# Optimization experiments

Hardware: AMD Instinct MI355X
Metric: run time of the kernel (lower is better)

## Reference

```python
import jax, jax.numpy as jnp
import numpy as np

EPS = 1e-5

@jax.custom_vjp
def sign_ste(x):
    # binarize to {-1, +1}; sign(0) maps to +1 as in most binary-net impls
    return jnp.where(x >= 0, 1.0, -1.0).astype(x.dtype)

def _sign_fwd(x):
    return sign_ste(x), x

def _sign_bwd(x, g):
    # straight-through estimator with hardtanh clipping
    return (g * (jnp.abs(x) <= 1.0).astype(g.dtype),)

sign_ste.defvjp(_sign_fwd, _sign_bwd)


def setup_inputs() -> dict:
    key = jax.random.key(0)
    k1, k2, k3 = jax.random.split(key, 3)
    N, Cin, Cout = 65536, 1024, 1024
    return {
        "x": jax.random.normal(k1, (N, Cin), dtype=jnp.float32),
        "gamma": jnp.ones((Cin,), dtype=jnp.float32),
        "beta": jnp.zeros((Cin,), dtype=jnp.float32),
        "W": jax.random.normal(k2, (Cout, Cin), dtype=jnp.float32) * 0.03,
        "b": jnp.zeros((Cout,), dtype=jnp.float32),
        "scale": jnp.ones((Cout,), dtype=jnp.float32),
        "alpha": jnp.float32(0.25),
    }


def reference(x, gamma, beta, W, b, scale, alpha):
    # 1) BatchNorm1d centering (training-mode batch statistics over nodes)
    mu = jnp.mean(x, axis=0)
    var = jnp.var(x, axis=0)
    xh = (x - mu) * jax.lax.rsqrt(var + EPS) * gamma + beta
    # 2) STE binarize activations
    xq = sign_ste(xh)
    # 3) binary linear: sign(W) GEMM + bias  -> [N, Cout]
    wq = sign_ste(W)
    y = jnp.einsum('nc,oc->no', xq, wq) + b
    # 4) learned per-channel rescale
    y = y * scale
    # 5) PReLU
    return jnp.where(y > 0, y, alpha * y)
```

## Files before the change

kernel.cpp:

```cpp
#include <hip/hip_runtime.h>
#include <stdint.h>
#include <math.h>

#define NROWS 65536
#define CIN   1024
#define COUT  1024
#define BN_EPS 1e-5


static constexpr size_t OFF_PSUM = 0;
static constexpr size_t OFF_PSQ  = 4ull * 1024 * 1024;
static constexpr size_t OFF_MU   = 8ull * 1024 * 1024;
static constexpr size_t OFF_INV  = 8ull * 1024 * 1024 + 4096;
static constexpr size_t OFF_WB   = 9ull * 1024 * 1024;
static constexpr size_t OFF_AB   = 10ull * 1024 * 1024;

typedef uint64_t u64x2 __attribute__((ext_vector_type(2)));
typedef uint32_t u32x4 __attribute__((ext_vector_type(4)));

__global__ __launch_bounds__(256) void k_stats_partial(
    const float* __restrict__ x, double* __restrict__ psum, double* __restrict__ psq) {
  int tid = threadIdx.x;
  size_t r0 = (size_t)blockIdx.x * 128;
  const float4* xp = (const float4*)x + r0 * 256 + tid;
  double s0 = 0, s1 = 0, s2 = 0, s3 = 0;
  double q0 = 0, q1 = 0, q2 = 0, q3 = 0;
  for (int r = 0; r < 128; r += 8) {
    float4 v[8];
#pragma unroll
    for (int u = 0; u < 8; ++u) v[u] = xp[(size_t)(r + u) * 256];
#pragma unroll
    for (int u = 0; u < 8; ++u) {
      double a = (double)v[u].x, b = (double)v[u].y;
      double c = (double)v[u].z, d = (double)v[u].w;
      s0 += a; q0 = fma(a, a, q0);
      s1 += b; q1 = fma(b, b, q1);
      s2 += c; q2 = fma(c, c, q2);
      s3 += d; q3 = fma(d, d, q3);
    }
  }
  size_t base = (size_t)blockIdx.x * CIN + (size_t)tid * 4;
  double2* ps = (double2*)(psum + base);
  ps[0] = make_double2(s0, s1);
  ps[1] = make_double2(s2, s3);
  double2* pq = (double2*)(psq + base);
  pq[0] = make_double2(q0, q1);
  pq[1] = make_double2(q2, q3);
}

__global__ __launch_bounds__(256) void k_stats_final(
    const double* __restrict__ psum, const double* __restrict__ psq,
    float* __restrict__ mu, float* __restrict__ inv) {
  __shared__ double sd[16][16];
  __shared__ double sq[16][16];
  int tid = threadIdx.x;
  int cl = tid & 15;
  int g  = tid >> 4;
  int col = blockIdx.x * 16 + cl;
  double s = 0, q = 0;
  for (int i = 0; i < 32; ++i) {
    size_t chunk = (size_t)(g * 32 + i);
    s += psum[chunk * CIN + col];
    q += psq [chunk * CIN + col];
  }
  sd[g][cl] = s;
  sq[g][cl] = q;
  __syncthreads();
  if (tid < 16) {
    s = 0; q = 0;
#pragma unroll
    for (int i = 0; i < 16; ++i) { s += sd[i][tid]; q += sq[i][tid]; }
    double mean = s / (double)NROWS;
    double var  = q / (double)NROWS - mean * mean;
    int c = blockIdx.x * 16 + tid;
    mu[c]  = (float)mean;
    inv[c] = (float)(1.0 / sqrt(var + (double)BN_EPS));
  }
}

__global__ __launch_bounds__(256) void k_binarize_x(
    const float* __restrict__ x, const float* __restrict__ mu,
    const float* __restrict__ inv, const float* __restrict__ gamma,
    const float* __restrict__ beta, uint64_t* __restrict__ Abits) {
  int tid = threadIdx.x, lane = tid & 63, wv = tid >> 6;
  float4 M  = ((const float4*)mu)[tid];
  float4 I  = ((const float4*)inv)[tid];
  float4 G  = ((const float4*)gamma)[tid];
  float4 Bt = ((const float4*)beta)[tid];
  size_t n0 = (size_t)blockIdx.x * 8;
  const float4* xp = (const float4*)x + n0 * 256 + tid;
  for (int r = 0; r < 8; ++r) {
    float4 v = xp[(size_t)r * 256];
    float h0 = ((v.x - M.x) * I.x) * G.x + Bt.x;
    float h1 = ((v.y - M.y) * I.y) * G.y + Bt.y;
    float h2 = ((v.z - M.z) * I.z) * G.z + Bt.z;
    float h3 = ((v.w - M.w) * I.w) * G.w + Bt.w;
    uint64_t b0 = __ballot(h0 >= 0.0f);
    uint64_t b1 = __ballot(h1 >= 0.0f);
    uint64_t b2 = __ballot(h2 >= 0.0f);
    uint64_t b3 = __ballot(h3 >= 0.0f);
    uint64_t t0 = b0, t1 = b1;
    if (lane == 1) { t0 = b2; t1 = b3; }
    if (lane < 2) {
      u64x2 val; val.x = t0; val.y = t1;
      *(u64x2*)(Abits + (n0 + r) * 16 + wv * 4 + lane * 2) = val;
    }
  }
}

__global__ __launch_bounds__(256) void k_binarize_w(
    const float* __restrict__ W, uint64_t* __restrict__ Wbits) {
  int tid = threadIdx.x, lane = tid & 63, wv = tid >> 6;
  size_t o0 = (size_t)blockIdx.x * 8;
  const float4* wp = (const float4*)W + o0 * 256 + tid;
  for (int r = 0; r < 8; ++r) {
    float4 v = wp[(size_t)r * 256];
    uint64_t b0 = __ballot(v.x >= 0.0f);
    uint64_t b1 = __ballot(v.y >= 0.0f);
    uint64_t b2 = __ballot(v.z >= 0.0f);
    uint64_t b3 = __ballot(v.w >= 0.0f);
    uint64_t t0 = b0, t1 = b1;
    if (lane == 1) { t0 = b2; t1 = b3; }
    if (lane < 2) {
      u64x2 val; val.x = t0; val.y = t1;
      *(u64x2*)(Wbits + (o0 + r) * 16 + wv * 4 + lane * 2) = val;
    }
  }
}

#define K5_ROWS 128
__global__ __launch_bounds__(256) void k_bingemm(
    const uint32_t* __restrict__ Abits, const uint32_t* __restrict__ Wbits,
    const float* __restrict__ bias, const float* __restrict__ scale,
    const float* __restrict__ alphaPtr, float* __restrict__ out) {
  __shared__ uint32_t tile[K5_ROWS * 32];
  int tid = threadIdx.x;
  int o = blockIdx.x * 256 + tid;
  size_t n0 = (size_t)blockIdx.y * K5_ROWS;

  {
    const u32x4* src = (const u32x4*)(Abits + n0 * 32);
    u32x4* dst = (u32x4*)tile;
#pragma unroll
    for (int i = 0; i < 4; ++i) dst[i * 256 + tid] = src[i * 256 + tid];
  }

  u32x4 B[8];
  const u32x4* wp = (const u32x4*)(Wbits + (size_t)o * 32);
#pragma unroll
  for (int j = 0; j < 8; ++j) B[j] = wp[j];

  float alpha = alphaPtr[0];
  float sc = scale[o];
  float c2 = -2.0f * sc;
  float c1 = (1024.0f + bias[o]) * sc;

  __syncthreads();

  float* op = out + n0 * COUT + o;
  for (int r = 0; r < K5_ROWS; ++r) {
    const u32x4* A = (const u32x4*)(tile + r * 32);
    int d0 = 0, d1 = 0, d2 = 0, d3 = 0;
#pragma unroll
    for (int j = 0; j < 8; ++j) {
      u32x4 a = A[j];
      d0 += __builtin_popcount(a.x ^ B[j].x);
      d1 += __builtin_popcount(a.y ^ B[j].y);
      d2 += __builtin_popcount(a.z ^ B[j].z);
      d3 += __builtin_popcount(a.w ^ B[j].w);
    }
    int d = (d0 + d1) + (d2 + d3);
    float y = fmaf((float)d, c2, c1);
    *op = y > 0.0f ? y : alpha * y;
    op += COUT;
  }
}

extern "C" void kernel_launch(void* const* d_in, const int* in_sizes, int n_in,
                              void* d_out, int out_size, void* d_ws, size_t ws_size,
                              hipStream_t stream) {
  const float* x     = (const float*)d_in[0];
  const float* gamma = (const float*)d_in[1];
  const float* beta  = (const float*)d_in[2];
  const float* W     = (const float*)d_in[3];
  const float* b     = (const float*)d_in[4];
  const float* scale = (const float*)d_in[5];
  const float* alpha = (const float*)d_in[6];
  float* out = (float*)d_out;

  char* ws = (char*)d_ws;
  double*   psum  = (double*)(ws + OFF_PSUM);
  double*   psq   = (double*)(ws + OFF_PSQ);
  float*    mu    = (float*)(ws + OFF_MU);
  float*    inv   = (float*)(ws + OFF_INV);
  uint64_t* Wbits = (uint64_t*)(ws + OFF_WB);
  uint64_t* Abits = (uint64_t*)(ws + OFF_AB);

  k_stats_partial<<<dim3(NROWS / 128), 256, 0, stream>>>(x, psum, psq);
  k_stats_final<<<dim3(CIN / 16), 256, 0, stream>>>(psum, psq, mu, inv);
  k_binarize_w<<<dim3(COUT / 8), 256, 0, stream>>>(W, Wbits);
  k_binarize_x<<<dim3(NROWS / 8), 256, 0, stream>>>(x, mu, inv, gamma, beta, Abits);
  k_bingemm<<<dim3(COUT / 256, NROWS / K5_ROWS), 256, 0, stream>>>(
      (const uint32_t*)Abits, (const uint32_t*)Wbits, b, scale, alpha, out);
}
```

Before: 594.1 us.

## Replace XOR-popcount binary GEMM with int8 MFMA GEMM on ±1 bytes

Binarized activations and weights are now stored as int8 ±1 values instead of packed bits. The GEMM runs on int8 MFMA 16x16x64 instructions, using 128x128 block tiles, direct global-to-LDS loads and an XOR-swizzled shared layout. This replaces the scalar popcount loop, which was ALU-bound. The trade-off is eight times more traffic for the binarized operands (64 MB for A), and the stats kernel now uses smaller row chunks, which doubles the number of partial sums.

```diff
diff --git a/kernel.cpp b/kernel.cpp
--- a/kernel.cpp
+++ b/kernel.cpp
@@ -7,25 +7,29 @@
 #define COUT  1024
 #define BN_EPS 1e-5
 
-
 static constexpr size_t OFF_PSUM = 0;
-static constexpr size_t OFF_PSQ  = 4ull * 1024 * 1024;
-static constexpr size_t OFF_MU   = 8ull * 1024 * 1024;
-static constexpr size_t OFF_INV  = 8ull * 1024 * 1024 + 4096;
-static constexpr size_t OFF_WB   = 9ull * 1024 * 1024;
-static constexpr size_t OFF_AB   = 10ull * 1024 * 1024;
-
-typedef uint64_t u64x2 __attribute__((ext_vector_type(2)));
-typedef uint32_t u32x4 __attribute__((ext_vector_type(4)));
+static constexpr size_t OFF_PSQ  = 8ull  * 1024 * 1024;
+static constexpr size_t OFF_MU   = 16ull * 1024 * 1024;
+static constexpr size_t OFF_INV  = 16ull * 1024 * 1024 + 4096;
+static constexpr size_t OFF_W8   = 17ull * 1024 * 1024;
+static constexpr size_t OFF_A8   = 24ull * 1024 * 1024;
+
+typedef int i32x4 __attribute__((ext_vector_type(4)));
+
+__device__ __forceinline__ void gload_lds16(const void* g, void* l) {
+  __builtin_amdgcn_global_load_lds(
+      (const __attribute__((address_space(1))) uint32_t*)g,
+      (__attribute__((address_space(3))) uint32_t*)l, 16, 0, 0);
+}
 
 __global__ __launch_bounds__(256) void k_stats_partial(
     const float* __restrict__ x, double* __restrict__ psum, double* __restrict__ psq) {
   int tid = threadIdx.x;
-  size_t r0 = (size_t)blockIdx.x * 128;
+  size_t r0 = (size_t)blockIdx.x * 64;
   const float4* xp = (const float4*)x + r0 * 256 + tid;
   double s0 = 0, s1 = 0, s2 = 0, s3 = 0;
   double q0 = 0, q1 = 0, q2 = 0, q3 = 0;
-  for (int r = 0; r < 128; r += 8) {
+  for (int r = 0; r < 64; r += 8) {
     float4 v[8];
 #pragma unroll
     for (int u = 0; u < 8; ++u) v[u] = xp[(size_t)(r + u) * 256];
@@ -58,8 +62,8 @@
   int g  = tid >> 4;
   int col = blockIdx.x * 16 + cl;
   double s = 0, q = 0;
-  for (int i = 0; i < 32; ++i) {
-    size_t chunk = (size_t)(g * 32 + i);
+  for (int i = 0; i < 64; ++i) {
+    size_t chunk = (size_t)(g * 64 + i);
     s += psum[chunk * CIN + col];
     q += psq [chunk * CIN + col];
   }
@@ -81,8 +85,8 @@
 __global__ __launch_bounds__(256) void k_binarize_x(
     const float* __restrict__ x, const float* __restrict__ mu,
     const float* __restrict__ inv, const float* __restrict__ gamma,
-    const float* __restrict__ beta, uint64_t* __restrict__ Abits) {
-  int tid = threadIdx.x, lane = tid & 63, wv = tid >> 6;
+    const float* __restrict__ beta, uint32_t* __restrict__ A8) {
+  int tid = threadIdx.x;
   float4 M  = ((const float4*)mu)[tid];
   float4 I  = ((const float4*)inv)[tid];
   float4 G  = ((const float4*)gamma)[tid];
@@ -95,84 +99,95 @@
     float h1 = ((v.y - M.y) * I.y) * G.y + Bt.y;
     float h2 = ((v.z - M.z) * I.z) * G.z + Bt.z;
     float h3 = ((v.w - M.w) * I.w) * G.w + Bt.w;
-    uint64_t b0 = __ballot(h0 >= 0.0f);
-    uint64_t b1 = __ballot(h1 >= 0.0f);
-    uint64_t b2 = __ballot(h2 >= 0.0f);
-    uint64_t b3 = __ballot(h3 >= 0.0f);
-    uint64_t t0 = b0, t1 = b1;
-    if (lane == 1) { t0 = b2; t1 = b3; }
-    if (lane < 2) {
-      u64x2 val; val.x = t0; val.y = t1;
-      *(u64x2*)(Abits + (n0 + r) * 16 + wv * 4 + lane * 2) = val;
-    }
+    uint32_t p = (h0 >= 0.0f ? 0x01u : 0xFFu)
+               | ((h1 >= 0.0f ? 0x01u : 0xFFu) << 8)
+               | ((h2 >= 0.0f ? 0x01u : 0xFFu) << 16)
+               | ((h3 >= 0.0f ? 0x01u : 0xFFu) << 24);
+    A8[(n0 + r) * 256 + tid] = p;
   }
 }
 
 __global__ __launch_bounds__(256) void k_binarize_w(
-    const float* __restrict__ W, uint64_t* __restrict__ Wbits) {
-  int tid = threadIdx.x, lane = tid & 63, wv = tid >> 6;
+    const float* __restrict__ W, uint32_t* __restrict__ W8) {
+  int tid = threadIdx.x;
   size_t o0 = (size_t)blockIdx.x * 8;
   const float4* wp = (const float4*)W + o0 * 256 + tid;
   for (int r = 0; r < 8; ++r) {
     float4 v = wp[(size_t)r * 256];
-    uint64_t b0 = __ballot(v.x >= 0.0f);
-    uint64_t b1 = __ballot(v.y >= 0.0f);
-    uint64_t b2 = __ballot(v.z >= 0.0f);
-    uint64_t b3 = __ballot(v.w >= 0.0f);
-    uint64_t t0 = b0, t1 = b1;
-    if (lane == 1) { t0 = b2; t1 = b3; }
-    if (lane < 2) {
-      u64x2 val; val.x = t0; val.y = t1;
-      *(u64x2*)(Wbits + (o0 + r) * 16 + wv * 4 + lane * 2) = val;
-    }
-  }
-}
-
-#define K5_ROWS 128
-__global__ __launch_bounds__(256) void k_bingemm(
-    const uint32_t* __restrict__ Abits, const uint32_t* __restrict__ Wbits,
+    uint32_t p = (v.x >= 0.0f ? 0x01u : 0xFFu)
+               | ((v.y >= 0.0f ? 0x01u : 0xFFu) << 8)
+               | ((v.z >= 0.0f ? 0x01u : 0xFFu) << 16)
+               | ((v.w >= 0.0f ? 0x01u : 0xFFu) << 24);
+    W8[(o0 + r) * 256 + tid] = p;
+  }
+}
+
+__global__ __launch_bounds__(256) void k_mmi8(
+    const int8_t* __restrict__ A8, const int8_t* __restrict__ W8,
     const float* __restrict__ bias, const float* __restrict__ scale,
     const float* __restrict__ alphaPtr, float* __restrict__ out) {
-  __shared__ uint32_t tile[K5_ROWS * 32];
-  int tid = threadIdx.x;
-  int o = blockIdx.x * 256 + tid;
-  size_t n0 = (size_t)blockIdx.y * K5_ROWS;
-
-  {
-    const u32x4* src = (const u32x4*)(Abits + n0 * 32);
-    u32x4* dst = (u32x4*)tile;
-#pragma unroll
-    for (int i = 0; i < 4; ++i) dst[i * 256 + tid] = src[i * 256 + tid];
-  }
-
-  u32x4 B[8];
-  const u32x4* wp = (const u32x4*)(Wbits + (size_t)o * 32);
-#pragma unroll
-  for (int j = 0; j < 8; ++j) B[j] = wp[j];
+  __shared__ uint8_t As[128 * 128];
+  __shared__ uint8_t Bs[128 * 128];
+  int tid  = threadIdx.x;
+  int lane = tid & 63, wv = tid >> 6;
+  int wr = wv >> 1, wc = wv & 1;
+  size_t n0 = (size_t)blockIdx.y * 128;
+  int c0 = blockIdx.x * 128;
+
+  i32x4 acc[4][4] = {};
+
+  int rsub = tid >> 3;
+  int swzc = ((tid & 7) ^ (rsub & 7)) << 4;
+  const int8_t* Asrc = A8 + (n0 + (size_t)rsub) * 1024 + swzc;
+  const int8_t* Bsrc = W8 + ((size_t)c0 + rsub) * 1024 + swzc;
+
+  for (int t = 0; t < 8; ++t) {
+#pragma unroll
+    for (int i = 0; i < 4; ++i) {
+      gload_lds16(Asrc + (size_t)i * 32 * 1024 + t * 128, &As[i * 4096 + wv * 1024]);
+      gload_lds16(Bsrc + (size_t)i * 32 * 1024 + t * 128, &Bs[i * 4096 + wv * 1024]);
+    }
+    __syncthreads();
+
+#pragma unroll
+    for (int kk = 0; kk < 2; ++kk) {
+      i32x4 af[4], bf[4];
+#pragma unroll
+      for (int m = 0; m < 4; ++m) {
+        int row = wr * 64 + m * 16 + (lane & 15);
+        int col = (kk * 64 + ((lane >> 4) << 4)) ^ ((lane & 7) << 4);
+        af[m] = *(const i32x4*)&As[row * 128 + col];
+      }
+#pragma unroll
+      for (int n = 0; n < 4; ++n) {
+        int row = wc * 64 + n * 16 + (lane & 15);
+        int col = (kk * 64 + ((lane >> 4) << 4)) ^ ((lane & 7) << 4);
+        bf[n] = *(const i32x4*)&Bs[row * 128 + col];
+      }
+#pragma unroll
+      for (int m = 0; m < 4; ++m)
+#pragma unroll
+        for (int n = 0; n < 4; ++n)
+          acc[m][n] = __builtin_amdgcn_mfma_i32_16x16x64_i8(af[m], bf[n], acc[m][n], 0, 0, 0);
+    }
+    __syncthreads();
+  }
 
   float alpha = alphaPtr[0];
-  float sc = scale[o];
-  float c2 = -2.0f * sc;
-  float c1 = (1024.0f + bias[o]) * sc;
-
-  __syncthreads();
-
-  float* op = out + n0 * COUT + o;
-  for (int r = 0; r < K5_ROWS; ++r) {
-    const u32x4* A = (const u32x4*)(tile + r * 32);
-    int d0 = 0, d1 = 0, d2 = 0, d3 = 0;
-#pragma unroll
-    for (int j = 0; j < 8; ++j) {
-      u32x4 a = A[j];
-      d0 += __builtin_popcount(a.x ^ B[j].x);
-      d1 += __builtin_popcount(a.y ^ B[j].y);
-      d2 += __builtin_popcount(a.z ^ B[j].z);
-      d3 += __builtin_popcount(a.w ^ B[j].w);
-    }
-    int d = (d0 + d1) + (d2 + d3);
-    float y = fmaf((float)d, c2, c1);
-    *op = y > 0.0f ? y : alpha * y;
-    op += COUT;
+#pragma unroll
+  for (int n = 0; n < 4; ++n) {
+    int col = c0 + wc * 64 + n * 16 + (lane & 15);
+    float b  = bias[col];
+    float sc = scale[col];
+#pragma unroll
+    for (int m = 0; m < 4; ++m) {
+      size_t rbase = n0 + (size_t)wr * 64 + m * 16 + ((lane >> 4) << 2);
+#pragma unroll
+      for (int r = 0; r < 4; ++r) {
+        float y = ((float)acc[m][n][r] + b) * sc;
+        out[(rbase + r) * COUT + col] = y > 0.0f ? y : alpha * y;
+      }
+    }
   }
 }
 
@@ -189,17 +204,17 @@
   float* out = (float*)d_out;
 
   char* ws = (char*)d_ws;
-  double*   psum  = (double*)(ws + OFF_PSUM);
-  double*   psq   = (double*)(ws + OFF_PSQ);
-  float*    mu    = (float*)(ws + OFF_MU);
-  float*    inv   = (float*)(ws + OFF_INV);
-  uint64_t* Wbits = (uint64_t*)(ws + OFF_WB);
-  uint64_t* Abits = (uint64_t*)(ws + OFF_AB);
-
-  k_stats_partial<<<dim3(NROWS / 128), 256, 0, stream>>>(x, psum, psq);
+  double*   psum = (double*)(ws + OFF_PSUM);
+  double*   psq  = (double*)(ws + OFF_PSQ);
+  float*    mu   = (float*)(ws + OFF_MU);
+  float*    inv  = (float*)(ws + OFF_INV);
+  uint32_t* W8   = (uint32_t*)(ws + OFF_W8);
+  uint32_t* A8   = (uint32_t*)(ws + OFF_A8);
+
+  k_stats_partial<<<dim3(NROWS / 64), 256, 0, stream>>>(x, psum, psq);
   k_stats_final<<<dim3(CIN / 16), 256, 0, stream>>>(psum, psq, mu, inv);
-  k_binarize_w<<<dim3(COUT / 8), 256, 0, stream>>>(W, Wbits);
-  k_binarize_x<<<dim3(NROWS / 8), 256, 0, stream>>>(x, mu, inv, gamma, beta, Abits);
-  k_bingemm<<<dim3(COUT / 256, NROWS / K5_ROWS), 256, 0, stream>>>(
-      (const uint32_t*)Abits, (const uint32_t*)Wbits, b, scale, alpha, out);
-}
+  k_binarize_w<<<dim3(COUT / 8), 256, 0, stream>>>(W, W8);
+  k_binarize_x<<<dim3(NROWS / 8), 256, 0, stream>>>(x, mu, inv, gamma, beta, A8);
+  k_mmi8<<<dim3(COUT / 128, NROWS / 128), 256, 0, stream>>>(
+      (const int8_t*)A8, (const int8_t*)W8, b, scale, alpha, out);
+}
```

After: 615.7 us. 3.6% more time.
